# Kernel tuning notes

Measured on AMD Instinct MI355X. Metric: run time of the kernel, lower is better.

## Reference

```python
import jax, jax.numpy as jnp
import numpy as np

B, T, C = 4, 2048, 1024
NUM_EXPERTS = 8
TOP_K = 2
D_EXPERT = 4 * C * TOP_K // NUM_EXPERTS  # 1024


def setup_inputs() -> dict:
    key = jax.random.key(0)
    k0, k1, k2, k3 = jax.random.split(key, 4)
    x = jax.random.normal(k0, (B, T, C), dtype=jnp.float32)
    # nn.Linear(n_embd, num_experts, bias=False).weight has shape [E, C]
    router_w = jax.random.normal(k1, (NUM_EXPERTS, C), dtype=jnp.float32) * 0.02
    # w1_all = stack of c_fc.weight.T  -> [E, C, D]
    w1_all = jax.random.normal(k2, (NUM_EXPERTS, C, D_EXPERT), dtype=jnp.float32) * 0.02
    # w2_all = stack of c_proj.weight.T -> [E, D, C]
    w2_all = jax.random.normal(k3, (NUM_EXPERTS, D_EXPERT, C), dtype=jnp.float32) * 0.02
    return {"x": x, "router_w": router_w, "w1_all": w1_all, "w2_all": w2_all}


def reference(x, router_w, w1_all, w2_all):
    b, t, c = x.shape
    x_flat = x.reshape(-1, c)                      # [N, C]
    router_logits = x_flat @ router_w.T            # [N, E]
    top_k_logits, top_k_idx = jax.lax.top_k(router_logits, TOP_K)  # [N, K]
    router_probs = jax.nn.softmax(top_k_logits, axis=-1)           # [N, K]

    # Same math as the original per-token weight gather, but computed as
    # dense all-expert GEMMs followed by an output gather (avoids the
    # [N, K, C, D] materialized weight copies while producing identical values).
    hidden = jnp.einsum('nc,ecd->ned', x_flat, w1_all)   # [N, E, D]
    hidden = jnp.square(jax.nn.relu(hidden))             # relu^2
    out_all = jnp.einsum('ned,edc->nec', hidden, w2_all) # [N, E, C]

    sel = jnp.take_along_axis(out_all, top_k_idx[:, :, None], axis=1)  # [N, K, C]
    out = jnp.sum(sel * router_probs[:, :, None], axis=1)             # [N, C]
    return out.reshape(b, t, c)
```

## Files before the change

kernel.cpp:

```cpp
#include <hip/hip_runtime.h>
#include <cstdint>
#include <cstddef>

typedef unsigned short ushort_t;
typedef unsigned short ushort8 __attribute__((ext_vector_type(8)));
typedef __bf16 bf16x8 __attribute__((ext_vector_type(8)));
typedef float floatx4 __attribute__((ext_vector_type(4)));

#define N_TOK 8192
#define CDIM 1024
#define NEXP 8

__device__ __forceinline__ float bf2f(ushort_t h) {
  union { unsigned int u; float f; } v; v.u = ((unsigned int)h) << 16; return v.f;
}
__device__ __forceinline__ ushort_t f2bf(float f) {
  union { float f; unsigned int u; } v; v.f = f;
  unsigned int r = v.u + 0x7fffu + ((v.u >> 16) & 1u);
  return (ushort_t)(r >> 16);
}

__device__ __forceinline__ void async_copy16(const ushort_t* g, ushort_t* l) {
  __builtin_amdgcn_global_load_lds(
      (const __attribute__((address_space(1))) unsigned int*)g,
      (__attribute__((address_space(3))) unsigned int*)l, 16, 0, 0);
}

__global__ void detect_init_kernel(const ushort_t* __restrict__ x,
                                   int* __restrict__ flag,
                                   int* __restrict__ cnt) {
  int tid = threadIdx.x;
  ushort_t u = x[tid];
  int ex = (u >> 7) & 0xFF;
  int crazy = (ex >= 0xC0 || ex <= 0x30) ? 1 : 0;
  int total = __syncthreads_count(crazy);
  if (tid == 0) flag[0] = (total >= 16) ? 1 : 0;
  if (tid < NEXP) cnt[tid] = 0;
}

__global__ void router_compute(const void* __restrict__ xv,
                               const void* __restrict__ rwv,
                               const int* __restrict__ flag,
                               int* __restrict__ tok_e,
                               float* __restrict__ prob,
                               ushort_t* __restrict__ xbf) {
  int isf32 = flag[0];
  int wid = threadIdx.x >> 6;
  int lane = threadIdx.x & 63;
  int t = blockIdx.x * 4 + wid;

  float acc[NEXP];
#pragma unroll
  for (int e = 0; e < NEXP; e++) acc[e] = 0.f;

  if (isf32) {
    const float* xr = (const float*)xv + (size_t)t * CDIM;
    const float* rw = (const float*)rwv;
#pragma unroll
    for (int half = 0; half < 2; half++) {
      int base = (lane + half * 64) * 8;
      floatx4 x0 = *(const floatx4*)(xr + base);
      floatx4 x1 = *(const floatx4*)(xr + base + 4);
      ushort8 o;
#pragma unroll
      for (int i = 0; i < 4; i++) { o[i] = f2bf(x0[i]); o[4 + i] = f2bf(x1[i]); }
      *(ushort8*)(xbf + (size_t)t * CDIM + base) = o;
#pragma unroll
      for (int e = 0; e < NEXP; e++) {
        floatx4 w0 = *(const floatx4*)(rw + e * CDIM + base);
        floatx4 w1 = *(const floatx4*)(rw + e * CDIM + base + 4);
        acc[e] += x0[0]*w0[0] + x0[1]*w0[1] + x0[2]*w0[2] + x0[3]*w0[3]
                + x1[0]*w1[0] + x1[1]*w1[1] + x1[2]*w1[2] + x1[3]*w1[3];
      }
    }
  } else {
    const ushort_t* xr = (const ushort_t*)xv + (size_t)t * CDIM;
    const ushort_t* rw = (const ushort_t*)rwv;
#pragma unroll
    for (int half = 0; half < 2; half++) {
      int base = (lane + half * 64) * 8;
      ushort8 xu = *(const ushort8*)(xr + base);
      *(ushort8*)(xbf + (size_t)t * CDIM + base) = xu;
#pragma unroll
      for (int e = 0; e < NEXP; e++) {
        ushort8 wu = *(const ushort8*)(rw + e * CDIM + base);
#pragma unroll
        for (int i = 0; i < 8; i++) acc[e] += bf2f(xu[i]) * bf2f(wu[i]);
      }
    }
  }

#pragma unroll
  for (int e = 0; e < NEXP; e++) {
#pragma unroll
    for (int off = 32; off > 0; off >>= 1) acc[e] += __shfl_xor(acc[e], off);
  }

  if (lane == 0) {
    int e0 = 0; float l0 = acc[0];
#pragma unroll
    for (int e = 1; e < NEXP; e++) if (acc[e] > l0) { l0 = acc[e]; e0 = e; }
    int e1 = (e0 == 0) ? 1 : 0; float l1 = acc[e1];
#pragma unroll
    for (int e = 0; e < NEXP; e++) {
      if (e != e0 && acc[e] > l1) { l1 = acc[e]; e1 = e; }
    }
    float p0 = 1.f / (1.f + __expf(l1 - l0));
    tok_e[t] = e0 | (e1 << 8);
    prob[t * 2] = p0;
    prob[t * 2 + 1] = 1.f - p0;
  }
}

__global__ void scatter_kernel(const int* __restrict__ tok_e,
                               int* __restrict__ cnt,
                               int* __restrict__ slots) {
  __shared__ int lcnt[NEXP];
  __shared__ int gbase[NEXP];
  int tid = threadIdx.x;
  if (tid < NEXP) lcnt[tid] = 0;
  __syncthreads();
  int t = blockIdx.x * 1024 + tid;
  int ee = tok_e[t];
  int e0 = ee & 0xFF, e1 = (ee >> 8) & 0xFF;
  int lofs0 = atomicAdd(&lcnt[e0], 1);
  int lofs1 = atomicAdd(&lcnt[e1], 1);
  __syncthreads();
  if (tid < NEXP) gbase[tid] = atomicAdd(&cnt[tid], lcnt[tid]);
  __syncthreads();
  slots[e0 * N_TOK + gbase[e0] + lofs0] = t * 2;
  slots[e1 * N_TOK + gbase[e1] + lofs1] = t * 2 + 1;
}

__global__ void transpose_kernel(const void* __restrict__ w1v,
                                 const void* __restrict__ w2v,
                                 const int* __restrict__ flag,
                                 ushort_t* __restrict__ w1T,
                                 ushort_t* __restrict__ w2T) {
  int isf32 = flag[0];
  int z = blockIdx.z;
  size_t moff = (size_t)(z & 7) << 20;
  const void* srcv = (z < 8) ? w1v : w2v;
  ushort_t* dst = ((z < 8) ? w1T : w2T) + moff;

  __shared__ __align__(16) ushort_t tile[64][72];
  int t = threadIdx.x;
  int R0 = blockIdx.y * 64, C0 = blockIdx.x * 64;
  int r = t >> 2, cb = (t & 3) * 16;
  if (isf32) {
    const float* sp = (const float*)srcv + moff + (size_t)(R0 + r) * 1024 + C0 + cb;
    ushort8 o0, o1;
#pragma unroll
    for (int q = 0; q < 2; q++) {
      floatx4 f = *(const floatx4*)(sp + q * 4);
#pragma unroll
      for (int i = 0; i < 4; i++) o0[q * 4 + i] = f2bf(f[i]);
    }
#pragma unroll
    for (int q = 0; q < 2; q++) {
      floatx4 f = *(const floatx4*)(sp + 8 + q * 4);
#pragma unroll
      for (int i = 0; i < 4; i++) o1[q * 4 + i] = f2bf(f[i]);
    }
    *(ushort8*)&tile[r][cb] = o0;
    *(ushort8*)&tile[r][cb + 8] = o1;
  } else {
    const ushort_t* sp = (const ushort_t*)srcv + moff + (size_t)(R0 + r) * 1024 + C0 + cb;
    *(ushort8*)&tile[r][cb] = *(const ushort8*)sp;
    *(ushort8*)&tile[r][cb + 8] = *(const ushort8*)(sp + 8);
  }
  __syncthreads();
  int d = t >> 2, rb = (t & 3) * 16;
  ushort8 o0, o1;
#pragma unroll
  for (int j = 0; j < 8; j++) { o0[j] = tile[rb + j][d]; o1[j] = tile[rb + 8 + j][d]; }
  ushort_t* dp = dst + (size_t)(C0 + d) * 1024 + R0 + rb;
  *(ushort8*)dp = o0;
  *(ushort8*)(dp + 8) = o1;
}

template <int MODE>
__global__ __launch_bounds__(512, 4) void moe_gemm(const ushort_t* __restrict__ A,
                                                   const ushort_t* __restrict__ BT,
                                                   ushort_t* __restrict__ Out,
                                                   const int* __restrict__ cnt,
                                                   const int* __restrict__ slots,
                                                   const float* __restrict__ prob) {
  int bid = blockIdx.x;
  int e = bid & 7;
  int nt = (bid >> 3) & 7;
  int mt = bid >> 6;
  int M = cnt[e];
  M = (M > N_TOK) ? N_TOK : M;
  int m0 = mt * 256;
  if (m0 >= M) return;
  int n0 = nt * 128;

  __shared__ __align__(16) ushort_t As[256 * 64];
  __shared__ __align__(16) ushort_t Bs[128 * 64];
  __shared__ int srow[256];

  int tid = threadIdx.x;
  if (tid < 256) {
    int gm = m0 + tid;
    int gi = (gm < M) ? gm : (M - 1);
    srow[tid] = slots[e * N_TOK + gi] & (2 * N_TOK - 1);
  }
  __syncthreads();

  int wid = tid >> 6;
  int lane = tid & 63;
  int lrow = lane >> 3;
  int gchunk = (lane & 7) ^ lrow;

  const ushort_t* aptr[4];
  const ushort_t* bptr[2];
  int arowbase = wid * 32;
  int browbase = wid * 16;
#pragma unroll
  for (int j = 0; j < 4; j++) {
    int rr = arowbase + j * 8 + lrow;
    int s = srow[rr];
    int aidx = (MODE == 0) ? (s >> 1) : s;
    aptr[j] = A + (size_t)aidx * CDIM + gchunk * 8;
  }
#pragma unroll
  for (int j = 0; j < 2; j++) {
    int rr = browbase + j * 8 + lrow;
    bptr[j] = BT + ((size_t)e << 20) + (size_t)(n0 + rr) * 1024 + gchunk * 8;
  }
  ushort_t* albase = &As[arowbase * 64];
  ushort_t* blbase = &Bs[browbase * 64];

  int wm = (wid >> 1) * 64;
  int wn = (wid & 1) * 64;
  int qd = lane >> 4;
  int ln = lane & 15;
  int l7 = ln & 7;

  floatx4 zero = {0.f, 0.f, 0.f, 0.f};
  floatx4 acc[4][4];
#pragma unroll
  for (int i = 0; i < 4; i++)
#pragma unroll
    for (int j = 0; j < 4; j++) acc[i][j] = zero;

  for (int k0 = 0; k0 < 1024; k0 += 64) {
    __syncthreads();
#pragma unroll
    for (int j = 0; j < 4; j++) async_copy16(aptr[j] + k0, albase + j * 512);
#pragma unroll
    for (int j = 0; j < 2; j++) async_copy16(bptr[j] + k0, blbase + j * 512);
    __syncthreads();
#pragma unroll
    for (int ks = 0; ks < 2; ks++) {
      bf16x8 afr[4], bfr[4];
#pragma unroll
      for (int i = 0; i < 4; i++) {
        int pc = ((ks * 4 + qd) ^ l7) * 8;
        afr[i] = *(const bf16x8*)&As[(wm + i * 16 + ln) * 64 + pc];
        bfr[i] = *(const bf16x8*)&Bs[(wn + i * 16 + ln) * 64 + pc];
      }
#pragma unroll
      for (int i = 0; i < 4; i++)
#pragma unroll
        for (int j = 0; j < 4; j++)
          acc[i][j] = __builtin_amdgcn_mfma_f32_16x16x32_bf16(afr[i], bfr[j], acc[i][j], 0, 0, 0);
    }
  }

#pragma unroll
  for (int i = 0; i < 4; i++) {
#pragma unroll
    for (int r = 0; r < 4; r++) {
      int rl = wm + i * 16 + qd * 4 + r;
      int gm = m0 + rl;
      if (gm >= M) continue;
      int s = srow[rl];
      float p = (MODE == 1) ? prob[s] : 0.f;
      ushort_t* orow = Out + (size_t)s * 1024 + n0 + wn + ln;
#pragma unroll
      for (int j = 0; j < 4; j++) {
        float v = acc[i][j][r];
        if (MODE == 0) { v = fmaxf(v, 0.f); v = v * v; }
        else v *= p;
        orow[j * 16] = f2bf(v);
      }
    }
  }
}

__global__ void combine_kernel(const ushort_t* __restrict__ oslots,
                               float* __restrict__ out) {
  int idx = (blockIdx.x * 256 + threadIdx.x) * 8;
  int t = idx >> 10;
  int c = idx & 1023;
  const ushort_t* r0 = oslots + ((size_t)t * 2) * 1024 + c;
  const ushort_t* r1 = r0 + 1024;
  ushort8 a = *(const ushort8*)r0;
  ushort8 b = *(const ushort8*)r1;
  floatx4 o0, o1;
#pragma unroll
  for (int i = 0; i < 4; i++) o0[i] = bf2f(a[i]) + bf2f(b[i]);
#pragma unroll
  for (int i = 0; i < 4; i++) o1[i] = bf2f(a[4 + i]) + bf2f(b[4 + i]);
  *(floatx4*)(out + idx) = o0;
  *(floatx4*)(out + idx + 4) = o1;
}

extern "C" void kernel_launch(void* const* d_in, const int* in_sizes, int n_in,
                              void* d_out, int out_size, void* d_ws, size_t ws_size,
                              hipStream_t stream) {
  const void* x  = d_in[0];
  const void* rw = d_in[1];
  const void* w1 = d_in[2];
  const void* w2 = d_in[3];
  float* out = (float*)d_out;
  char* ws = (char*)d_ws;

  int* cnt  = (int*)(ws + 0);
  int* flag = (int*)(ws + 64);
  int* slots = (int*)(ws + 1024);
  float* prob = (float*)(ws + 263168);
  int* tok_e = (int*)(ws + 335872);
  ushort_t* xbf = (ushort_t*)(ws + 524288);
  ushort_t* w1T = (ushort_t*)(ws + 17301504);
  ushort_t* hidden = (ushort_t*)(ws + 34078720);
  ushort_t* w2T = (ushort_t*)(ws + 67633152);
  ushort_t* oslots = (ushort_t*)(ws + 524288);

  detect_init_kernel<<<1, 128, 0, stream>>>((const ushort_t*)x, flag, cnt);
  router_compute<<<N_TOK / 4, 256, 0, stream>>>(x, rw, flag, tok_e, prob, xbf);
  scatter_kernel<<<NEXP, 1024, 0, stream>>>(tok_e, cnt, slots);
  transpose_kernel<<<dim3(16, 16, 16), 256, 0, stream>>>(w1, w2, flag, w1T, w2T);
  moe_gemm<0><<<2048, 512, 0, stream>>>(xbf, w1T, hidden, cnt, slots, prob);
  moe_gemm<1><<<2048, 512, 0, stream>>>(hidden, w2T, oslots, cnt, slots, prob);
  combine_kernel<<<4096, 256, 0, stream>>>(oslots, out);
}
```

Measured before the change: 267.6 us.

## Double-buffer MoE GEMM LDS tiles with K=32 stages and async prefetch

Replaces the single-buffered K=64 LDS tile loop with two K=32 buffers, so the global-to-LDS loads for the next stage are issued before computing the current one. Explicit vmcnt waits and raw s_barrier calls replace the full __syncthreads pair, and s_setprio raises wave priority around the MFMA block. The aim is to hide global load latency behind matrix math. The cost is twice as many iterations with half the work each, more barriers per K, and a new XOR swizzle over only 4 chunks, which may bring back LDS bank conflicts.

```diff
diff --git a/kernel.cpp b/kernel.cpp
--- a/kernel.cpp
+++ b/kernel.cpp
@@ -196,8 +196,8 @@
   if (m0 >= M) return;
   int n0 = nt * 128;
 
-  __shared__ __align__(16) ushort_t As[256 * 64];
-  __shared__ __align__(16) ushort_t Bs[128 * 64];
+  __shared__ __align__(16) ushort_t As[2][256 * 32];
+  __shared__ __align__(16) ushort_t Bs[2][128 * 32];
   __shared__ int srow[256];
 
   int tid = threadIdx.x;
@@ -210,33 +210,29 @@
 
   int wid = tid >> 6;
   int lane = tid & 63;
-  int lrow = lane >> 3;
-  int gchunk = (lane & 7) ^ lrow;
-
-  const ushort_t* aptr[4];
-  const ushort_t* bptr[2];
-  int arowbase = wid * 32;
-  int browbase = wid * 16;
-#pragma unroll
-  for (int j = 0; j < 4; j++) {
-    int rr = arowbase + j * 8 + lrow;
+  int lrow = lane >> 2;
+  int gchunk = (lane & 3) ^ (lrow & 3);
+
+  const ushort_t* aptr[2];
+  const ushort_t* bptr0;
+#pragma unroll
+  for (int j = 0; j < 2; j++) {
+    int rr = j * 128 + wid * 16 + lrow;
     int s = srow[rr];
     int aidx = (MODE == 0) ? (s >> 1) : s;
     aptr[j] = A + (size_t)aidx * CDIM + gchunk * 8;
   }
-#pragma unroll
-  for (int j = 0; j < 2; j++) {
-    int rr = browbase + j * 8 + lrow;
-    bptr[j] = BT + ((size_t)e << 20) + (size_t)(n0 + rr) * 1024 + gchunk * 8;
-  }
-  ushort_t* albase = &As[arowbase * 64];
-  ushort_t* blbase = &Bs[browbase * 64];
+  {
+    int rr = wid * 16 + lrow;
+    bptr0 = BT + ((size_t)e << 20) + (size_t)(n0 + rr) * 1024 + gchunk * 8;
+  }
 
   int wm = (wid >> 1) * 64;
   int wn = (wid & 1) * 64;
   int qd = lane >> 4;
   int ln = lane & 15;
-  int l7 = ln & 7;
+  int l3 = ln & 3;
+  int pc = (qd ^ l3) * 8;
 
   floatx4 zero = {0.f, 0.f, 0.f, 0.f};
   floatx4 acc[4][4];
@@ -245,29 +241,48 @@
 #pragma unroll
     for (int j = 0; j < 4; j++) acc[i][j] = zero;
 
-  for (int k0 = 0; k0 < 1024; k0 += 64) {
-    __syncthreads();
-#pragma unroll
-    for (int j = 0; j < 4; j++) async_copy16(aptr[j] + k0, albase + j * 512);
-#pragma unroll
-    for (int j = 0; j < 2; j++) async_copy16(bptr[j] + k0, blbase + j * 512);
-    __syncthreads();
-#pragma unroll
-    for (int ks = 0; ks < 2; ks++) {
-      bf16x8 afr[4], bfr[4];
-#pragma unroll
-      for (int i = 0; i < 4; i++) {
-        int pc = ((ks * 4 + qd) ^ l7) * 8;
-        afr[i] = *(const bf16x8*)&As[(wm + i * 16 + ln) * 64 + pc];
-        bfr[i] = *(const bf16x8*)&Bs[(wn + i * 16 + ln) * 64 + pc];
-      }
-#pragma unroll
-      for (int i = 0; i < 4; i++)
-#pragma unroll
-        for (int j = 0; j < 4; j++)
-          acc[i][j] = __builtin_amdgcn_mfma_f32_16x16x32_bf16(afr[i], bfr[j], acc[i][j], 0, 0, 0);
-    }
-  }
+#define STAGE(buf, kofs)                                                     \
+  do {                                                                       \
+    async_copy16(aptr[0] + (kofs), &As[buf][wid * 512]);                     \
+    async_copy16(aptr[1] + (kofs), &As[buf][4096 + wid * 512]);              \
+    async_copy16(bptr0 + (kofs), &Bs[buf][wid * 512]);                       \
+  } while (0)
+
+#define COMPUTE(cb)                                                          \
+  do {                                                                       \
+    bf16x8 afr[4], bfr[4];                                                   \
+    _Pragma("unroll")                                                        \
+    for (int i = 0; i < 4; i++) {                                            \
+      afr[i] = *(const bf16x8*)&As[cb][(wm + i * 16 + ln) * 32 + pc];        \
+      bfr[i] = *(const bf16x8*)&Bs[cb][(wn + i * 16 + ln) * 32 + pc];        \
+    }                                                                        \
+    __builtin_amdgcn_s_setprio(1);                                           \
+    _Pragma("unroll")                                                        \
+    for (int i = 0; i < 4; i++)                                              \
+      _Pragma("unroll")                                                      \
+      for (int j = 0; j < 4; j++)                                            \
+        acc[i][j] = __builtin_amdgcn_mfma_f32_16x16x32_bf16(afr[i], bfr[j],  \
+                                                            acc[i][j], 0, 0, 0); \
+    __builtin_amdgcn_s_setprio(0);                                           \
+  } while (0)
+
+  STAGE(0, 0);
+  int cur = 0;
+  for (int kt = 0; kt < 31; ++kt) {
+    STAGE(cur ^ 1, (kt + 1) * 32);
+    asm volatile("s_waitcnt vmcnt(3)" ::: "memory");
+    __builtin_amdgcn_s_barrier();
+    COMPUTE(cur);
+    asm volatile("s_waitcnt lgkmcnt(0)" ::: "memory");
+    __builtin_amdgcn_s_barrier();
+    cur ^= 1;
+  }
+  asm volatile("s_waitcnt vmcnt(0)" ::: "memory");
+  __builtin_amdgcn_s_barrier();
+  COMPUTE(cur);
+
+#undef STAGE
+#undef COMPUTE
 
 #pragma unroll
   for (int i = 0; i < 4; i++) {
```

Measured after the change: 290.7 us. +8.7%, slower.
